# Kernel tuning notes

Hardware: AMD Instinct MI355X
Metric: run time of the kernel (lower is better)

## Reference

```python
import jax, jax.numpy as jnp
import numpy as np
from jax import lax

EPS = 1e-15
DIM = 8          # per-head dim
HEADS = 32       # in_channels // dim
HEADQ = 2 * HEADS  # qkv branch + one multi-scale branch concatenated
BN_EPS = 1e-5

def conv2d(x, w, groups=1, pad=0):
    return lax.conv_general_dilated(
        x, w, (1, 1), [(pad, pad), (pad, pad)],
        feature_group_count=groups,
        dimension_numbers=('NCHW', 'OIHW', 'NCHW'))

def l2n(x):
    return x / (jnp.linalg.norm(x, axis=-1, keepdims=True) + EPS)

def setup_inputs() -> dict:
    key = jax.random.key(0)
    ks = jax.random.split(key, 6)
    B, C, H, W = 8, 256, 56, 56
    sc = lambda k, shape, s=0.05: (jax.random.normal(k, shape, jnp.float32) * s)
    return {
        'x': jax.random.normal(ks[0], (B, C, H, W), jnp.float32),
        'w_qkv': sc(ks[1], (768, 256, 1, 1)),
        'w_dw': sc(ks[2], (768, 1, 5, 5)),
        'w_pw': sc(ks[3], (768, 8, 1, 1)),
        'pos_enc': sc(ks[4], (1, 512, H, W), 0.02),
        'ones_scale1': jnp.ones((), jnp.float32),
        'bn_gamma': jnp.ones((8,), jnp.float32),
        'bn_beta': jnp.zeros((8,), jnp.float32),
        'bn_mean': jnp.zeros((8,), jnp.float32),
        'bn_var': jnp.ones((8,), jnp.float32),
        'w_proj': sc(ks[5], (256, 512, 1, 1)),
        'pbn_gamma': jnp.ones((256,), jnp.float32),
        'pbn_beta': jnp.zeros((256,), jnp.float32),
        'pbn_mean': jnp.zeros((256,), jnp.float32),
        'pbn_var': jnp.ones((256,), jnp.float32),
    }

def reference(x, w_qkv, w_dw, w_pw, pos_enc, ones_scale1,
              bn_gamma, bn_beta, bn_mean, bn_var,
              w_proj, pbn_gamma, pbn_beta, pbn_mean, pbn_var):
    B, _, H, W = x.shape
    N = H * W
    # qkv projection (1x1 conv, no norm/act)
    qkv = conv2d(x, w_qkv)                                  # (B,768,H,W)
    # multi-scale aggregation: depthwise 5x5 then grouped 1x1 (groups=3*heads)
    tmp = conv2d(qkv, w_dw, groups=768, pad=2)
    tmp = conv2d(tmp, w_pw, groups=96)
    ms = jnp.concatenate([qkv, tmp], axis=1)                # (B,1536,H,W)
    # qt_attention
    t = ms.reshape(B, HEADQ, 3 * DIM, N).transpose(0, 1, 3, 2)  # (B,64,N,24)
    q, k, v = t[..., :DIM], t[..., DIM:2 * DIM], t[..., 2 * DIM:]
    pos = pos_enc.reshape(1, HEADQ, DIM, N).transpose(0, 1, 3, 2)  # (1,64,N,8)
    k = k + pos
    # double-normalized squared kernel features
    q = l2n(l2n(q) ** 2)
    k = l2n(l2n(k) ** 2)
    ones = ones_scale1 * jnp.ones((B, HEADQ, N, 1), q.dtype)
    q = jnp.concatenate([q, ones], axis=-1)                 # (B,64,N,9)
    k = jnp.concatenate([k, ones], axis=-1)
    v1 = jnp.concatenate([v, jnp.ones((B, HEADQ, N, 1), v.dtype)], axis=-1)
    kv = jnp.einsum('bhnc,bhnd->bhcd', k, v1)               # (B,64,9,9)
    out = jnp.einsum('bhnc,bhcd->bhnd', q, kv)              # (B,64,N,9)
    out = out[..., :-1] / (out[..., -1:] + EPS)
    # feature-map residual branch (no-mask path): BN(eval)+GELU over v
    fm = v1[..., :-1].reshape(B * HEADQ, H, W, DIM)          # channels-last BN over DIM
    fm = (fm - bn_mean) * (bn_gamma / jnp.sqrt(bn_var + BN_EPS)) + bn_beta
    fm = jax.nn.gelu(fm, approximate=False).reshape(B, HEADQ, N, DIM)
    out = out + fm
    out = out.transpose(0, 1, 3, 2).reshape(B, HEADQ * DIM, H, W)  # (B,512,H,W)
    # proj: 1x1 conv + bn2d (eval), no act
    out = conv2d(out, w_proj)                                # (B,256,H,W)
    out = (out - pbn_mean[:, None, None]) * (pbn_gamma[:, None, None]
           / jnp.sqrt(pbn_var[:, None, None] + BN_EPS)) + pbn_beta[:, None, None]
    return out
```

## Files before the change

kernel.cpp:

```cpp
#include <hip/hip_runtime.h>
#include <cstdint>

#define NPIX 3136
#define HGT 56
#define WID 56
#define NPAD 3200

typedef __bf16 bf16x8 __attribute__((ext_vector_type(8)));
typedef __bf16 bf16x4 __attribute__((ext_vector_type(4)));
typedef float  f32x4  __attribute__((ext_vector_type(4)));

typedef const __attribute__((address_space(1))) unsigned int* gptr_t;
typedef __attribute__((address_space(3))) unsigned int* lptr_t;

__device__ __forceinline__ void gload_lds16(const __bf16* g, __bf16* l) {
    __builtin_amdgcn_global_load_lds((gptr_t)(const void*)g, (lptr_t)(void*)l, 16, 0, 0);
}

__device__ __forceinline__ float fast_gelu(float x) {
    float y = 0.7978845608f * x * (1.f + 0.044715f * x * x);
    float t = __expf(-2.f * fabsf(y));
    float th = (1.f - t) * __builtin_amdgcn_rcpf(1.f + t);
    th = copysignf(th, y);
    return 0.5f * x * (1.f + th);
}

__global__ __launch_bounds__(256) void wcvt(
    const float* __restrict__ wq, const float* __restrict__ wp,
    __bf16* __restrict__ oq, __bf16* __restrict__ op)
{
    int i = blockIdx.x * 256 + threadIdx.x;
    if (i < 768 * 256) oq[i] = (__bf16)wq[i];
    if (i < 256 * 512) op[i] = (__bf16)wp[i];
}

__global__ __launch_bounds__(256) void xpose_cvt(
    const float* __restrict__ x, __bf16* __restrict__ xT)
{
    __shared__ float t[32][33];
    const int n0 = blockIdx.x * 32;
    const int k0 = blockIdx.y * 32;
    const int b  = blockIdx.z;
    const int tid = threadIdx.x;
    const int ln = tid & 31, lk = tid >> 5;
    #pragma unroll
    for (int r = 0; r < 4; ++r) {
        int n = n0 + ln, k = k0 + lk + r * 8;
        t[lk + r * 8][ln] = (n < NPIX) ? x[((size_t)b * 256 + k) * NPIX + n] : 0.f;
    }
    __syncthreads();
    const int nr = tid >> 3, kc = (tid & 7) * 4;
    bf16x4 o;
    #pragma unroll
    for (int i = 0; i < 4; ++i) o[i] = (__bf16)t[kc + i][nr];
    *(bf16x4*)&xT[((size_t)b * NPAD + n0 + nr) * 256 + k0 + kc] = o;
}

template<int BN, int MODE>
__global__ __launch_bounds__(256) void gemm1x1(
    const __bf16* __restrict__ A,
    const __bf16* __restrict__ Bm,
    void* __restrict__ Cout,
    const int M, const int K, const int N, const int NP,
    const int NT, const int MT,
    const float* __restrict__ bn_g, const float* __restrict__ bn_b,
    const float* __restrict__ bn_m, const float* __restrict__ bn_v)
{
    constexpr int NFRAG = BN / 32;
    __shared__ __bf16 As[128 * 32];
    __shared__ __bf16 Bs[BN * 32];
    const int tid = threadIdx.x;

    const int F = blockIdx.x;
    const int gpb = MT * 8;
    const int A_ = F / gpb, R_ = F % gpb;
    const int mi = R_ >> 3, ci = R_ & 7;
    const int g_ = A_ * 8 + ci;
    const int n0 = (g_ % NT) * BN;
    const int b  = g_ / NT;
    const int m0 = mi * 128;

    const int lane = tid & 63, wid = tid >> 6;
    const int wr = wid >> 1, wc = wid & 1;
    const int lr = lane & 15, lk = (lane >> 4) * 8;

    f32x4 acc[4][NFRAG] = {};
    const __bf16* Ap = A + (size_t)m0 * K;
    const __bf16* Bp = Bm + ((size_t)b * NP + n0) * K;
    const int ar = tid >> 2, ac = (tid & 3) * 8;

    for (int k0 = 0; k0 < K; k0 += 32) {
        __syncthreads();
        gload_lds16(Ap + (size_t)ar * K + k0 + ac,          As + ar * 32 + ac);
        gload_lds16(Ap + (size_t)(ar + 64) * K + k0 + ac,   As + (ar + 64) * 32 + ac);
        #pragma unroll
        for (int i = 0; i < BN / 64; ++i)
            gload_lds16(Bp + (size_t)(ar + i * 64) * K + k0 + ac, Bs + (ar + i * 64) * 32 + ac);
        __syncthreads();

        bf16x8 af[4], bfr[NFRAG];
        #pragma unroll
        for (int i = 0; i < 4; ++i)
            af[i] = *(const bf16x8*)(As + (wr * 64 + i * 16 + lr) * 32 + lk);
        #pragma unroll
        for (int j = 0; j < NFRAG; ++j)
            bfr[j] = *(const bf16x8*)(Bs + (wc * (BN / 2) + j * 16 + lr) * 32 + lk);
        #pragma unroll
        for (int i = 0; i < 4; ++i)
            #pragma unroll
            for (int j = 0; j < NFRAG; ++j)
                acc[i][j] = __builtin_amdgcn_mfma_f32_16x16x32_bf16(af[i], bfr[j], acc[i][j], 0, 0, 0);
    }

    const int rbase = (lane >> 4) * 4;
    if (MODE == 0) {
        __bf16* C = (__bf16*)Cout + (size_t)b * M * N;
        #pragma unroll
        for (int i = 0; i < 4; ++i)
            #pragma unroll
            for (int r = 0; r < 4; ++r) {
                const int m = m0 + wr * 64 + i * 16 + rbase + r;
                #pragma unroll
                for (int j = 0; j < NFRAG; ++j) {
                    const int n = n0 + wc * (BN / 2) + j * 16 + lr;
                    if (n < N) C[(size_t)m * N + n] = (__bf16)acc[i][j][r];
                }
            }
    } else {
        float* C = (float*)Cout + (size_t)b * M * N;
        #pragma unroll
        for (int i = 0; i < 4; ++i)
            #pragma unroll
            for (int r = 0; r < 4; ++r) {
                const int m = m0 + wr * 64 + i * 16 + rbase + r;
                const float sc = bn_g[m] * rsqrtf(bn_v[m] + 1e-5f);
                const float mu = bn_m[m], bb = bn_b[m];
                #pragma unroll
                for (int j = 0; j < NFRAG; ++j) {
                    const int n = n0 + wc * (BN / 2) + j * 16 + lr;
                    if (n < N) C[(size_t)m * N + n] = (acc[i][j][r] - mu) * sc + bb;
                }
            }
    }
}

__global__ __launch_bounds__(256) void dw5x5(
    const __bf16* __restrict__ in, const float* __restrict__ w,
    __bf16* __restrict__ out)
{
    __shared__ float t[60 * 60];
    const int bc = blockIdx.x;
    const int c  = bc % 768;
    const __bf16* __restrict__ ip = in + (size_t)bc * NPIX;
    __bf16* __restrict__ op = out + (size_t)bc * NPIX;
    const int tid = threadIdx.x;

    for (int i = tid; i < 464; i += 256) {
        int y, x;
        if (i < 240)      { y = (i < 120) ? (i / 60) : (58 + (i - 120) / 60); x = i % 60; }
        else if (i < 352) { y = 2 + (i - 240) / 2; x = (i - 240) & 1; }
        else              { y = 2 + (i - 352) / 2; x = 58 + ((i - 352) & 1); }
        t[y * 60 + x] = 0.f;
    }
    for (int i = tid; i < 392; i += 256) {
        const int p = i * 8, y = p / 56, x = p % 56;
        bf16x8 v = *(const bf16x8*)&ip[p];
        float* d = &t[(y + 2) * 60 + x + 2];
        #pragma unroll
        for (int j = 0; j < 8; ++j) d[j] = (float)v[j];
    }
    float wv[25];
    #pragma unroll
    for (int j = 0; j < 25; ++j) wv[j] = w[c * 25 + j];
    __syncthreads();

    const int x  = tid & 63;
    const int y0 = (tid >> 6) * 14;
    if (x < WID) {
        float win[5][5];
        #pragma unroll
        for (int r = 0; r < 4; ++r)
            #pragma unroll
            for (int cc = 0; cc < 5; ++cc)
                win[r][cc] = t[(y0 + r) * 60 + x + cc];
        #pragma unroll
        for (int i = 0; i < 14; ++i) {
            #pragma unroll
            for (int cc = 0; cc < 5; ++cc)
                win[4][cc] = t[(y0 + i + 4) * 60 + x + cc];
            float s = 0.f;
            #pragma unroll
            for (int r = 0; r < 5; ++r)
                #pragma unroll
                for (int cc = 0; cc < 5; ++cc)
                    s += win[r][cc] * wv[r * 5 + cc];
            op[(y0 + i) * WID + x] = (__bf16)s;
            #pragma unroll
            for (int r = 0; r < 4; ++r)
                #pragma unroll
                for (int cc = 0; cc < 5; ++cc)
                    win[r][cc] = win[r + 1][cc];
        }
    }
}

__global__ __launch_bounds__(256) void pw_group(
    const __bf16* __restrict__ in, const float* __restrict__ w,
    __bf16* __restrict__ out)
{
    const int bg = blockIdx.x;
    const int g  = bg % 96;
    const size_t base = (size_t)(bg / 96) * 768 * NPIX + (size_t)(g * 8) * NPIX;
    const __bf16* __restrict__ ip = in + base;
    __bf16* __restrict__ op = out + base;

    float wv[64];
    #pragma unroll
    for (int l = 0; l < 64; ++l) wv[l] = w[(g * 8 + (l >> 3)) * 8 + (l & 7)];

    for (int oct = threadIdx.x; oct < 392; oct += 256) {
        const int p = oct * 8;
        float xi[8][8];
        #pragma unroll
        for (int i = 0; i < 8; ++i) {
            bf16x8 v = *(const bf16x8*)&ip[(size_t)i * NPIX + p];
            #pragma unroll
            for (int j = 0; j < 8; ++j) xi[i][j] = (float)v[j];
        }
        #pragma unroll
        for (int o = 0; o < 8; ++o) {
            bf16x8 ov;
            #pragma unroll
            for (int j = 0; j < 8; ++j) {
                float s = 0.f;
                #pragma unroll
                for (int i = 0; i < 8; ++i) s += wv[o * 8 + i] * xi[i][j];
                ov[j] = (__bf16)s;
            }
            *(bf16x8*)&op[(size_t)o * NPIX + p] = ov;
        }
    }
}

__global__ __launch_bounds__(256) void attn_kv4(
    const __bf16* __restrict__ qkvb, const __bf16* __restrict__ pwb,
    const float* __restrict__ pos, const float* __restrict__ s1p,
    float* __restrict__ kvpart)
{
    __shared__ __bf16 kl[4][9][256];
    __shared__ __bf16 vl[4][9][256];
    __shared__ float red[4][16][16];
    const int chunk = blockIdx.x;
    const int h = blockIdx.y, b = blockIdx.z;
    const __bf16* __restrict__ src = (h < 32)
        ? qkvb + ((size_t)b * 768 + h * 24) * NPIX
        : pwb  + ((size_t)b * 768 + (h - 32) * 24) * NPIX;
    const float* __restrict__ pp = pos + (size_t)(h * 8) * NPIX;
    const float s1 = s1p[0];
    const int tid = threadIdx.x, lane = tid & 63, wid = tid >> 6;
    const int tbase = chunk * 12;
    const int nt = (chunk == 3) ? 13 : 12;
    const int lr = lane & 15, g = lane >> 4;

    __bf16 (*K)[256] = kl[wid];
    __bf16 (*V)[256] = vl[wid];

    {
        bf16x4 s1q, oneq;
        #pragma unroll
        for (int j = 0; j < 4; ++j) { s1q[j] = (__bf16)s1; oneq[j] = (__bf16)1.0f; }
        *(bf16x4*)&K[8][lane * 4] = s1q;
        *(bf16x4*)&V[8][lane * 4] = oneq;
    }

    f32x4 acc = {};

    for (int r = wid; r * 4 < nt; r += 4) {
        const int T = min(4, nt - r * 4);
        if (lane < T * 16) {
            const int n = (tbase + r * 4) * 64 + lane * 4;
            bf16x4 kr[8], vr[8];
            f32x4 pr[8];
            #pragma unroll
            for (int c = 0; c < 8; ++c) {
                kr[c] = *(const bf16x4*)&src[(size_t)(8 + c) * NPIX + n];
                pr[c] = *(const f32x4*)&pp[(size_t)c * NPIX + n];
                vr[c] = *(const bf16x4*)&src[(size_t)(16 + c) * NPIX + n];
            }
            float k1[8][4];
            #pragma unroll
            for (int j = 0; j < 4; ++j) {
                float u[8], s2 = 0.f;
                #pragma unroll
                for (int c = 0; c < 8; ++c) {
                    float kk = (float)kr[c][j] + pr[c][j];
                    u[c] = kk * kk;
                    s2 += u[c] * u[c];
                }
                float inv = 1.f / (sqrtf(s2) + 1e-15f);
                #pragma unroll
                for (int c = 0; c < 8; ++c) k1[c][j] = u[c] * inv;
            }
            const int px  = lane * 4;
            const int tb  = px & ~63;
            const int oct = (px >> 3) & 7;
            const int sub = px & 7;
            #pragma unroll
            for (int c = 0; c < 8; ++c) {
                bf16x4 kq;
                #pragma unroll
                for (int j = 0; j < 4; ++j) kq[j] = (__bf16)k1[c][j];
                *(bf16x4*)&K[c][tb + ((oct ^ c) << 3) + sub] = kq;
                *(bf16x4*)&V[c][tb + ((oct ^ c) << 3) + sub] = vr[c];
            }
        }
        for (int t = 0; t < T; ++t) {
            #pragma unroll
            for (int s = 0; s < 2; ++s) {
                const int off = t * 64 + (((s * 4 + g) ^ (lr & 7)) << 3);
                bf16x8 a = *(const bf16x8*)&K[lr][off];
                bf16x8 bb = *(const bf16x8*)&V[lr][off];
                acc = __builtin_amdgcn_mfma_f32_16x16x32_bf16(a, bb, acc, 0, 0, 0);
            }
        }
    }

    #pragma unroll
    for (int r = 0; r < 4; ++r) red[wid][g * 4 + r][lr] = acc[r];
    __syncthreads();
    if (tid < 81) {
        const int c = tid / 9, d = tid % 9;
        kvpart[((size_t)chunk * 512 + b * 64 + h) * 81 + tid]
            = red[0][c][d] + red[1][c][d] + red[2][c][d] + red[3][c][d];
    }
}

__global__ __launch_bounds__(256) void attn_out6(
    const __bf16* __restrict__ qkvb, const __bf16* __restrict__ pwb,
    const float* __restrict__ kvpart,
    const float* __restrict__ bng, const float* __restrict__ bnb,
    const float* __restrict__ bnm, const float* __restrict__ bnv,
    const float* __restrict__ s1p, __bf16* __restrict__ attb)
{
    __shared__ float kvs[8 * 81];
    __shared__ __bf16 att[64 * 64];
    const int b = blockIdx.z;
    const int hq0 = blockIdx.y * 8;
    const int n0 = blockIdx.x * 64;
    const int tid = threadIdx.x, lane = tid & 63, wv_ = tid >> 6;
    const int n = n0 + lane;
    const float s1 = s1p[0];

    const int S = 512 * 81;
    for (int i = tid; i < 8 * 81; i += 256) {
        const size_t off = ((size_t)b * 64 + hq0) * 81 + i;
        kvs[i] = (kvpart[off] + kvpart[S + off])
               + (kvpart[2 * S + off] + kvpart[3 * S + off]);
    }
    __syncthreads();

    float bsc[8], bmu[8], bbe[8];
    #pragma unroll
    for (int d = 0; d < 8; ++d) {
        bsc[d] = bng[d] * rsqrtf(bnv[d] + 1e-5f);
        bmu[d] = bnm[d];
        bbe[d] = bnb[d];
    }

    #pragma unroll
    for (int hh = 0; hh < 2; ++hh) {
        const int hl = wv_ * 2 + hh;
        const int h = hq0 + hl;
        const __bf16* __restrict__ src = (h < 32)
            ? qkvb + ((size_t)b * 768 + h * 24) * NPIX
            : pwb  + ((size_t)b * 768 + (h - 32) * 24) * NPIX;
        const float* __restrict__ kvh = &kvs[hl * 81];

        float q1[9], s2 = 0.f;
        #pragma unroll
        for (int c = 0; c < 8; ++c) {
            float qq = (float)src[(size_t)c * NPIX + n];
            q1[c] = qq * qq;
            s2 += q1[c] * q1[c];
        }
        float inv = 1.f / (sqrtf(s2) + 1e-15f);
        #pragma unroll
        for (int c = 0; c < 8; ++c) q1[c] *= inv;
        q1[8] = s1;

        float den = 0.f;
        #pragma unroll
        for (int c = 0; c < 9; ++c) den += q1[c] * kvh[c * 9 + 8];
        const float invd = 1.f / (den + 1e-15f);

        bf16x8 o;
        #pragma unroll
        for (int d = 0; d < 8; ++d) {
            float num = 0.f;
            #pragma unroll
            for (int c = 0; c < 9; ++c) num += q1[c] * kvh[c * 9 + d];
            float v = (float)src[(size_t)(16 + d) * NPIX + n];
            float fmv = (v - bmu[d]) * bsc[d] + bbe[d];
            o[d] = (__bf16)(num * invd + fast_gelu(fmv));
        }
        *(bf16x8*)((char*)att + lane * 128 + ((hl * 16) ^ ((lane & 7) << 4))) = o;
    }
    __syncthreads();

    #pragma unroll
    for (int p = 0; p < 2; ++p) {
        const int px = p * 32 + (tid >> 3);
        const int s = tid & 7;
        bf16x8 o = *(const bf16x8*)((const char*)att + px * 128 + ((s * 16) ^ ((px & 7) << 4)));
        *(bf16x8*)&attb[((size_t)b * NPIX + n0 + px) * 512 + hq0 * 8 + s * 8] = o;
    }
}

extern "C" void kernel_launch(void* const* d_in, const int* in_sizes, int n_in,
                              void* d_out, int out_size, void* d_ws, size_t ws_size,
                              hipStream_t stream)
{
    const float* x      = (const float*)d_in[0];
    const float* w_qkv  = (const float*)d_in[1];
    const float* w_dw   = (const float*)d_in[2];
    const float* w_pw   = (const float*)d_in[3];
    const float* pos    = (const float*)d_in[4];
    const float* s1     = (const float*)d_in[5];
    const float* bng    = (const float*)d_in[6];
    const float* bnb    = (const float*)d_in[7];
    const float* bnm    = (const float*)d_in[8];
    const float* bnv    = (const float*)d_in[9];
    const float* w_proj = (const float*)d_in[10];
    const float* pg     = (const float*)d_in[11];
    const float* pb     = (const float*)d_in[12];
    const float* pm     = (const float*)d_in[13];
    const float* pv     = (const float*)d_in[14];
    float* out = (float*)d_out;

    char* w = (char*)d_ws;
    __bf16* xT    = (__bf16*)(w);
    __bf16* qkvb  = (__bf16*)(w + 13107200);
    __bf16* dwb   = (__bf16*)(w + 51642368);
    __bf16* pwb   = (__bf16*)(w + 90177536);
    __bf16* attb  = (__bf16*)(w + 128712704);
    float*  kvpart= (float*) (w + 154402816);
    __bf16* wq_bf = (__bf16*)(w + 155066368);
    __bf16* wp_bf = (__bf16*)(w + 155459584);

    wcvt<<<768, 256, 0, stream>>>(w_qkv, w_proj, wq_bf, wp_bf);
    xpose_cvt<<<dim3(100, 8, 8), 256, 0, stream>>>(x, xT);

    gemm1x1<128, 0><<<dim3(1200), 256, 0, stream>>>(
        wq_bf, xT, qkvb, 768, 256, NPIX, NPAD, 25, 6,
        nullptr, nullptr, nullptr, nullptr);

    dw5x5<<<dim3(8 * 768), 256, 0, stream>>>(qkvb, w_dw, dwb);
    pw_group<<<dim3(8 * 96), 256, 0, stream>>>(dwb, w_pw, pwb);

    attn_kv4<<<dim3(4, 64, 8), 256, 0, stream>>>(qkvb, pwb, pos, s1, kvpart);
    attn_out6<<<dim3(49, 8, 8), 256, 0, stream>>>(
        qkvb, pwb, kvpart, bng, bnb, bnm, bnv, s1, attb);

    gemm1x1<64, 1><<<dim3(784), 256, 0, stream>>>(
        wp_bf, attb, out, 256, 512, NPIX, NPIX, 49, 2,
        pg, pb, pm, pv);
}
```

Before: 130.3 us.

## Fuse depthwise 5x5 and grouped pointwise convs into one slab-tiled kernel

Replaces the separate depthwise 5x5 and grouped 1x1 kernels with a single kernel in which each block handles one 8-channel group over a 14-row slab with halo. The depthwise result stays in shared memory and feeds the pointwise step directly, which removes a full bf16 intermediate write and read of the 8x768x3136 tensor plus one launch. In exchange, halo rows are reloaded for each slab, the pointwise phase only keeps 98 of 256 threads busy, and the larger shared footprint may lower occupancy.

```diff
diff --git a/kernel.cpp b/kernel.cpp
--- a/kernel.cpp
+++ b/kernel.cpp
@@ -9,6 +9,7 @@
 typedef __bf16 bf16x8 __attribute__((ext_vector_type(8)));
 typedef __bf16 bf16x4 __attribute__((ext_vector_type(4)));
 typedef float  f32x4  __attribute__((ext_vector_type(4)));
+typedef float  f32x2  __attribute__((ext_vector_type(2)));
 
 typedef const __attribute__((address_space(1))) unsigned int* gptr_t;
 typedef __attribute__((address_space(3))) unsigned int* lptr_t;
@@ -144,57 +145,61 @@
     }
 }
 
-__global__ __launch_bounds__(256) void dw5x5(
-    const __bf16* __restrict__ in, const float* __restrict__ w,
-    __bf16* __restrict__ out)
-{
-    __shared__ float t[60 * 60];
-    const int bc = blockIdx.x;
-    const int c  = bc % 768;
-    const __bf16* __restrict__ ip = in + (size_t)bc * NPIX;
-    __bf16* __restrict__ op = out + (size_t)bc * NPIX;
+__global__ __launch_bounds__(256) void dwpw2(
+    const __bf16* __restrict__ in, const float* __restrict__ wdw,
+    const float* __restrict__ wpw, __bf16* __restrict__ out)
+{
+    __shared__ float  tin[8][18][60];
+    __shared__ __bf16 tdw[8][784];
+    __shared__ float  wdws[8][25];
+    __shared__ float  wpws[64];
+    const int slab = blockIdx.x, g = blockIdx.y, b = blockIdx.z;
+    const int y0 = slab * 14;
     const int tid = threadIdx.x;
-
-    for (int i = tid; i < 464; i += 256) {
-        int y, x;
-        if (i < 240)      { y = (i < 120) ? (i / 60) : (58 + (i - 120) / 60); x = i % 60; }
-        else if (i < 352) { y = 2 + (i - 240) / 2; x = (i - 240) & 1; }
-        else              { y = 2 + (i - 352) / 2; x = 58 + ((i - 352) & 1); }
-        t[y * 60 + x] = 0.f;
-    }
-    for (int i = tid; i < 392; i += 256) {
-        const int p = i * 8, y = p / 56, x = p % 56;
-        bf16x8 v = *(const bf16x8*)&ip[p];
-        float* d = &t[(y + 2) * 60 + x + 2];
-        #pragma unroll
-        for (int j = 0; j < 8; ++j) d[j] = (float)v[j];
-    }
-    float wv[25];
-    #pragma unroll
-    for (int j = 0; j < 25; ++j) wv[j] = w[c * 25 + j];
-    __syncthreads();
-
-    const int x  = tid & 63;
-    const int y0 = (tid >> 6) * 14;
-    if (x < WID) {
+    const __bf16* __restrict__ ip = in + ((size_t)b * 768 + g * 8) * NPIX;
+
+    for (int i = tid; i < 2160; i += 256)
+        ((f32x4*)tin)[i] = (f32x4){0.f, 0.f, 0.f, 0.f};
+    if (tid < 200) ((float*)wdws)[tid] = wdw[g * 200 + tid];
+    if (tid < 64)  wpws[tid] = wpw[g * 64 + tid];
+    __syncthreads();
+
+    for (int i = tid; i < 1008; i += 256) {
+        const int ch = i / 126, rem = i % 126;
+        const int yr = rem / 7, oct = rem % 7;
+        const int y = y0 + yr - 2;
+        if (y >= 0 && y < HGT) {
+            bf16x8 v = *(const bf16x8*)&ip[(size_t)ch * NPIX + y * WID + oct * 8];
+            float* d = &tin[ch][yr][2 + oct * 8];
+            #pragma unroll
+            for (int j = 0; j < 4; ++j)
+                *(f32x2*)&d[j * 2] = (f32x2){(float)v[j * 2], (float)v[j * 2 + 1]};
+        }
+    }
+    __syncthreads();
+
+    for (int task = tid; task < 448; task += 256) {
+        const int ch = task / 56, x = task % 56;
+        float wv[25];
+        #pragma unroll
+        for (int j = 0; j < 25; ++j) wv[j] = wdws[ch][j];
         float win[5][5];
         #pragma unroll
         for (int r = 0; r < 4; ++r)
             #pragma unroll
             for (int cc = 0; cc < 5; ++cc)
-                win[r][cc] = t[(y0 + r) * 60 + x + cc];
-        #pragma unroll
-        for (int i = 0; i < 14; ++i) {
+                win[r][cc] = tin[ch][r][x + cc];
+        for (int rr = 0; rr < 14; ++rr) {
             #pragma unroll
             for (int cc = 0; cc < 5; ++cc)
-                win[4][cc] = t[(y0 + i + 4) * 60 + x + cc];
+                win[4][cc] = tin[ch][rr + 4][x + cc];
             float s = 0.f;
             #pragma unroll
             for (int r = 0; r < 5; ++r)
                 #pragma unroll
                 for (int cc = 0; cc < 5; ++cc)
                     s += win[r][cc] * wv[r * 5 + cc];
-            op[(y0 + i) * WID + x] = (__bf16)s;
+            tdw[ch][rr * 56 + x] = (__bf16)s;
             #pragma unroll
             for (int r = 0; r < 4; ++r)
                 #pragma unroll
@@ -202,30 +207,17 @@
                     win[r][cc] = win[r + 1][cc];
         }
     }
-}
-
-__global__ __launch_bounds__(256) void pw_group(
-    const __bf16* __restrict__ in, const float* __restrict__ w,
-    __bf16* __restrict__ out)
-{
-    const int bg = blockIdx.x;
-    const int g  = bg % 96;
-    const size_t base = (size_t)(bg / 96) * 768 * NPIX + (size_t)(g * 8) * NPIX;
-    const __bf16* __restrict__ ip = in + base;
-    __bf16* __restrict__ op = out + base;
-
-    float wv[64];
-    #pragma unroll
-    for (int l = 0; l < 64; ++l) wv[l] = w[(g * 8 + (l >> 3)) * 8 + (l & 7)];
-
-    for (int oct = threadIdx.x; oct < 392; oct += 256) {
+    __syncthreads();
+
+    __bf16* __restrict__ op = out + ((size_t)b * 768 + g * 8) * NPIX + y0 * WID;
+    for (int oct = tid; oct < 98; oct += 256) {
         const int p = oct * 8;
         float xi[8][8];
         #pragma unroll
-        for (int i = 0; i < 8; ++i) {
-            bf16x8 v = *(const bf16x8*)&ip[(size_t)i * NPIX + p];
-            #pragma unroll
-            for (int j = 0; j < 8; ++j) xi[i][j] = (float)v[j];
+        for (int i2 = 0; i2 < 8; ++i2) {
+            bf16x8 v = *(const bf16x8*)&tdw[i2][p];
+            #pragma unroll
+            for (int j = 0; j < 8; ++j) xi[i2][j] = (float)v[j];
         }
         #pragma unroll
         for (int o = 0; o < 8; ++o) {
@@ -234,7 +226,7 @@
             for (int j = 0; j < 8; ++j) {
                 float s = 0.f;
                 #pragma unroll
-                for (int i = 0; i < 8; ++i) s += wv[o * 8 + i] * xi[i][j];
+                for (int i2 = 0; i2 < 8; ++i2) s += wpws[o * 8 + i2] * xi[i2][j];
                 ov[j] = (__bf16)s;
             }
             *(bf16x8*)&op[(size_t)o * NPIX + p] = ov;
@@ -440,12 +432,11 @@
     char* w = (char*)d_ws;
     __bf16* xT    = (__bf16*)(w);
     __bf16* qkvb  = (__bf16*)(w + 13107200);
-    __bf16* dwb   = (__bf16*)(w + 51642368);
-    __bf16* pwb   = (__bf16*)(w + 90177536);
-    __bf16* attb  = (__bf16*)(w + 128712704);
-    float*  kvpart= (float*) (w + 154402816);
-    __bf16* wq_bf = (__bf16*)(w + 155066368);
-    __bf16* wp_bf = (__bf16*)(w + 155459584);
+    __bf16* pwb   = (__bf16*)(w + 51642368);
+    __bf16* attb  = (__bf16*)(w + 90177536);
+    float*  kvpart= (float*) (w + 115867648);
+    __bf16* wq_bf = (__bf16*)(w + 116531200);
+    __bf16* wp_bf = (__bf16*)(w + 116924416);
 
     wcvt<<<768, 256, 0, stream>>>(w_qkv, w_proj, wq_bf, wp_bf);
     xpose_cvt<<<dim3(100, 8, 8), 256, 0, stream>>>(x, xT);
@@ -454,8 +445,7 @@
         wq_bf, xT, qkvb, 768, 256, NPIX, NPAD, 25, 6,
         nullptr, nullptr, nullptr, nullptr);
 
-    dw5x5<<<dim3(8 * 768), 256, 0, stream>>>(qkvb, w_dw, dwb);
-    pw_group<<<dim3(8 * 96), 256, 0, stream>>>(dwb, w_pw, pwb);
+    dwpw2<<<dim3(4, 96, 8), 256, 0, stream>>>(qkvb, w_dw, w_pw, pwb);
 
     attn_kv4<<<dim3(4, 64, 8), 256, 0, stream>>>(qkvb, pwb, pos, s1, kvpart);
     attn_out6<<<dim3(49, 8, 8), 256, 0, stream>>>(
```

Result: no change. 129.4 us (-0.7%).
